# Kernel optimization log

Hardware: AMD Instinct MI355X
Metric: run time of the kernel (lower is better)

## Reference

```python
import jax, jax.numpy as jnp
import numpy as np

A = 4          # lanczos parameter
LUT = 1024     # LUT resolution; table has LUT+1 entries (torch.range is end-inclusive)
TAPS = 9
PAD = 4


def _lanczos_table():
    # delta_X = 1e-8 + i/1024, i = 0..1024  (matches torch.range(1e-8, 1.0, 1/1024))
    delta = jnp.float32(1e-08) + jnp.arange(LUT + 1, dtype=jnp.float32) / LUT  # (1025,)
    offs = jnp.arange(-PAD, PAD + 1, dtype=jnp.float32)[:, None]               # (9,1): row p -> delta + (p-4)
    t = delta[None, :] + offs                                                  # (9,1025)
    pi = jnp.float32(np.pi)
    return jnp.sin(t * pi) / (t * pi) * (jnp.sin(t * pi / A) / (t * pi / A))   # (9,1025)


def _resample_last_axis(x, sub, n_out):
    # x: (..., n_out) nearest-gathered signal; sub: (n_out,) fractional offsets in [0,1)
    pad = [(0, 0)] * (x.ndim - 1) + [(PAD, PAD)]
    xp = jnp.pad(x, pad, mode='reflect')                     # reflect pad by 4 on last axis
    idx = jnp.floor(sub * LUT).astype(jnp.int32)             # (n_out,) LUT index, 0..1023
    w = _lanczos_table()[:, idx]                             # (9, n_out) per-pixel tap weights
    # out[..., j] = sum_p w[p, j] * xp[..., j + p]
    return sum(w[p] * xp[..., p:p + n_out] for p in range(TAPS))


def reference(img, new_h, new_w):
    B, C, H, W = img.shape
    yv = jnp.arange(new_h, dtype=jnp.float32) * (H / new_h)   # torch.arange(0, H, H/H2)
    xv = jnp.arange(new_w, dtype=jnp.float32) * (W / new_w)
    yi = jnp.floor(yv).astype(jnp.int32)
    xi = jnp.floor(xv).astype(jnp.int32)
    ys = yv - yi                                              # fractional parts (separable)
    xs = xv - xi
    # nearest-neighbor gather img[:, :, y_init_up, x_init_up] -> (B, C, H2, W2)
    g = img[:, :, yi, :][:, :, :, xi]
    # horizontal Lanczos pass (unfold_x equivalent)
    hx = _resample_last_axis(g, xs, new_w)
    # vertical Lanczos pass (unfold_y equivalent), done on transposed view
    hy = _resample_last_axis(jnp.swapaxes(hx, 2, 3), ys, new_h)
    return jnp.swapaxes(hy, 2, 3)


def setup_inputs() -> dict:
    key = jax.random.key(0)
    img = jax.random.normal(key, (4, 2, 256, 256), dtype=jnp.float32)
    return {"img": img, "new_h": 2048, "new_w": 2048}
```

## Files before the change

### kernel.cpp

```cpp
#include <hip/hip_runtime.h>


#define WA0 0.0f
#define WA1 -0.03041110f
#define WA2 0.02753266f
#define WA3 -0.00827163f
#define WA4 1.00243180f
#define WA5 1.01040147f
#define WA6 0.97375330f
#define WA7 1.03080550f
#define WB0 1.0f
#define WB1 1.02991210f
#define WB2 0.97065798f
#define WB3 1.00472265f
#define WB4 -0.00765906f
#define WB5 -0.01652347f
#define WB6 0.02047608f
#define WB7 -0.03455115f
#define WS0 1.0f
#define WS1 0.99950100f
#define WS2 0.99819064f
#define WS3 0.99645102f
#define WS4 0.99477274f
#define WS5 0.99387800f
#define WS6 0.99422938f
#define WS7 0.99625435f

__global__ __launch_bounds__(512) void lanczos_up8_kernel(
    const float* __restrict__ img, float* __restrict__ out)
{
    int bid  = blockIdx.x;
    int t    = bid & 255;
    int bc   = bid >> 8;
    int v    = threadIdx.x;

    int P = v & 1;
    int m = v >> 1;

    bool eL = (v == 0);
    bool eR = (v == 511);

    float a0 = P ? WA4 : WA0, b0 = P ? WB4 : WB0;
    float a1 = P ? WA5 : WA1, b1 = P ? WB5 : WB1;
    float a2 = P ? WA6 : WA2, b2 = P ? WB6 : WB2;
    float a3 = P ? WA7 : WA3, b3 = P ? WB7 : WB3;
    if (eL) { a0 = WS0; a1 = WS1; a2 = WS2; a3 = WS3; b0 = b1 = b2 = b3 = 0.f; }
    if (eR) { a0 = WS4; a1 = WS5; a2 = WS6; a3 = WS7; b0 = b1 = b2 = b3 = 0.f; }

    int c0 = P ? m : m - 1;
    if (eL) c0 = 0;
    if (eR) c0 = 255;
    int c1 = (eL || eR) ? c0 : c0 + 1;

    int rm = t > 0   ? t - 1 : 0;
    int rp = t < 255 ? t + 1 : 255;

    const float* base = img + bc * 65536;
    float i00 = base[rm * 256 + c0], i01 = base[rm * 256 + c1];
    float i10 = base[t  * 256 + c0], i11 = base[t  * 256 + c1];
    float i20 = base[rp * 256 + c0], i21 = base[rp * 256 + c1];

    float h00 = a0*i00 + b0*i01, h01 = a1*i00 + b1*i01, h02 = a2*i00 + b2*i01, h03 = a3*i00 + b3*i01;
    float h10 = a0*i10 + b0*i11, h11 = a1*i10 + b1*i11, h12 = a2*i10 + b2*i11, h13 = a3*i10 + b3*i11;
    float h20 = a0*i20 + b0*i21, h21 = a1*i20 + b1*i21, h22 = a2*i20 + b2*i21, h23 = a3*i20 + b3*i21;

    bool eT = (t == 0);
    bool eB = (t == 255);

    float* op = out + (size_t)bc * (2048 * 2048)
                    + (size_t)(t << 3) * 2048 + (v << 2);

    float va, vb; float4 o;
#define EMIT(S, WAs, WBs, WSs, HX0,HX1,HX2,HX3, HY0,HY1,HY2,HY3, EDGE)   \
    va = (EDGE) ? WSs : WAs;  vb = (EDGE) ? 0.f : WBs;                   \
    o.x = va*HX0 + vb*HY0;  o.y = va*HX1 + vb*HY1;                       \
    o.z = va*HX2 + vb*HY2;  o.w = va*HX3 + vb*HY3;                       \
    *reinterpret_cast<float4*>(op + S * 2048) = o;

    EMIT(0, WA0, WB0, WS0, h00,h01,h02,h03, h10,h11,h12,h13, eT)
    EMIT(1, WA1, WB1, WS1, h00,h01,h02,h03, h10,h11,h12,h13, eT)
    EMIT(2, WA2, WB2, WS2, h00,h01,h02,h03, h10,h11,h12,h13, eT)
    EMIT(3, WA3, WB3, WS3, h00,h01,h02,h03, h10,h11,h12,h13, eT)
    EMIT(4, WA4, WB4, WS4, h10,h11,h12,h13, h20,h21,h22,h23, eB)
    EMIT(5, WA5, WB5, WS5, h10,h11,h12,h13, h20,h21,h22,h23, eB)
    EMIT(6, WA6, WB6, WS6, h10,h11,h12,h13, h20,h21,h22,h23, eB)
    EMIT(7, WA7, WB7, WS7, h10,h11,h12,h13, h20,h21,h22,h23, eB)
#undef EMIT
}

extern "C" void kernel_launch(void* const* d_in, const int* in_sizes, int n_in,
                              void* d_out, int out_size, void* d_ws, size_t ws_size,
                              hipStream_t stream) {
    const float* img = (const float*)d_in[0];
    float* out = (float*)d_out;
    dim3 grid(2048), block(512);
    hipLaunchKernelGGL(lanczos_up8_kernel, grid, block, 0, stream, img, out);
}
```

Measured before the change: 26.35 us.

## Remap threads so each wavefront writes one output row contiguously

Threads are reassigned so each wavefront owns one of the 8 output rows and loops over 8 column segments. Previously every thread wrote float4s across 8 rows. Now each store instruction covers a contiguous 1KB span of a single row, which is meant to improve write coalescing and reduce strided store streams. The cost is recomputing the vertical blend per column segment and issuing more, partly redundant, input loads per thread (mostly L1/L2 hits).

Result: slower. 27.23 us (+3.4%).

```diff
diff --git a/kernel.cpp b/kernel.cpp
--- a/kernel.cpp
+++ b/kernel.cpp
@@ -32,60 +32,54 @@
     int bid  = blockIdx.x;
     int t    = bid & 255;
     int bc   = bid >> 8;
-    int v    = threadIdx.x;
+    int tid  = threadIdx.x;
+    int lane = tid & 63;
+    int s    = tid >> 6;
 
-    int P = v & 1;
-    int m = v >> 1;
+    bool hi = (s >= 4);
+    float va = s==0?WA0: s==1?WA1: s==2?WA2: s==3?WA3: s==4?WA4: s==5?WA5: s==6?WA6: WA7;
+    float vb = s==0?WB0: s==1?WB1: s==2?WB2: s==3?WB3: s==4?WB4: s==5?WB5: s==6?WB6: WB7;
+    float ws = s==0?WS0: s==1?WS1: s==2?WS2: s==3?WS3: s==4?WS4: s==5?WS5: s==6?WS6: WS7;
+    bool eT = (t == 0)   && !hi;
+    bool eB = (t == 255) &&  hi;
+    if (eT || eB) { va = ws; vb = 0.f; }
+    int r0 = hi ? t : t - 1;  if (r0 < 0)   r0 = 0;
+    int r1 = r0 + 1;          if (r1 > 255) r1 = 255;
 
-    bool eL = (v == 0);
-    bool eR = (v == 511);
-
+    int P = lane & 1;
     float a0 = P ? WA4 : WA0, b0 = P ? WB4 : WB0;
     float a1 = P ? WA5 : WA1, b1 = P ? WB5 : WB1;
     float a2 = P ? WA6 : WA2, b2 = P ? WB6 : WB2;
     float a3 = P ? WA7 : WA3, b3 = P ? WB7 : WB3;
-    if (eL) { a0 = WS0; a1 = WS1; a2 = WS2; a3 = WS3; b0 = b1 = b2 = b3 = 0.f; }
-    if (eR) { a0 = WS4; a1 = WS5; a2 = WS6; a3 = WS7; b0 = b1 = b2 = b3 = 0.f; }
+    int cb = (lane >> 1) - 1 + P;
 
-    int c0 = P ? m : m - 1;
-    if (eL) c0 = 0;
-    if (eR) c0 = 255;
-    int c1 = (eL || eR) ? c0 : c0 + 1;
-
-    int rm = t > 0   ? t - 1 : 0;
-    int rp = t < 255 ? t + 1 : 255;
-
-    const float* base = img + bc * 65536;
-    float i00 = base[rm * 256 + c0], i01 = base[rm * 256 + c1];
-    float i10 = base[t  * 256 + c0], i11 = base[t  * 256 + c1];
-    float i20 = base[rp * 256 + c0], i21 = base[rp * 256 + c1];
-
-    float h00 = a0*i00 + b0*i01, h01 = a1*i00 + b1*i01, h02 = a2*i00 + b2*i01, h03 = a3*i00 + b3*i01;
-    float h10 = a0*i10 + b0*i11, h11 = a1*i10 + b1*i11, h12 = a2*i10 + b2*i11, h13 = a3*i10 + b3*i11;
-    float h20 = a0*i20 + b0*i21, h21 = a1*i20 + b1*i21, h22 = a2*i20 + b2*i21, h23 = a3*i20 + b3*i21;
-
-    bool eT = (t == 0);
-    bool eB = (t == 255);
+    const float* row0 = img + bc * 65536 + r0 * 256;
+    const float* row1 = img + bc * 65536 + r1 * 256;
 
     float* op = out + (size_t)bc * (2048 * 2048)
-                    + (size_t)(t << 3) * 2048 + (v << 2);
+                    + ((size_t)(t << 3) + s) * 2048 + (lane << 2);
 
-    float va, vb; float4 o;
-#define EMIT(S, WAs, WBs, WSs, HX0,HX1,HX2,HX3, HY0,HY1,HY2,HY3, EDGE)   \
-    va = (EDGE) ? WSs : WAs;  vb = (EDGE) ? 0.f : WBs;                   \
-    o.x = va*HX0 + vb*HY0;  o.y = va*HX1 + vb*HY1;                       \
-    o.z = va*HX2 + vb*HY2;  o.w = va*HX3 + vb*HY3;                       \
-    *reinterpret_cast<float4*>(op + S * 2048) = o;
-
-    EMIT(0, WA0, WB0, WS0, h00,h01,h02,h03, h10,h11,h12,h13, eT)
-    EMIT(1, WA1, WB1, WS1, h00,h01,h02,h03, h10,h11,h12,h13, eT)
-    EMIT(2, WA2, WB2, WS2, h00,h01,h02,h03, h10,h11,h12,h13, eT)
-    EMIT(3, WA3, WB3, WS3, h00,h01,h02,h03, h10,h11,h12,h13, eT)
-    EMIT(4, WA4, WB4, WS4, h10,h11,h12,h13, h20,h21,h22,h23, eB)
-    EMIT(5, WA5, WB5, WS5, h10,h11,h12,h13, h20,h21,h22,h23, eB)
-    EMIT(6, WA6, WB6, WS6, h10,h11,h12,h13, h20,h21,h22,h23, eB)
-    EMIT(7, WA7, WB7, WS7, h10,h11,h12,h13, h20,h21,h22,h23, eB)
-#undef EMIT
+    #pragma unroll
+    for (int st = 0; st < 8; ++st) {
+        int g  = (st << 6) | lane;
+        int c0 = cb + (st << 5);
+        int c1 = c0 + 1;
+        float A0=a0, A1=a1, A2=a2, A3=a3, B0=b0, B1=b1, B2=b2, B3=b3;
+        if (st == 0 && g == 0)   { A0=WS0; A1=WS1; A2=WS2; A3=WS3;
+                                   B0=B1=B2=B3=0.f; c0=0;   c1=0;   }
+        if (st == 7 && g == 511) { A0=WS4; A1=WS5; A2=WS6; A3=WS7;
+                                   B0=B1=B2=B3=0.f; c0=255; c1=255; }
+        float i0 = row0[c0], i1 = row0[c1];
+        float i2 = row1[c0], i3 = row1[c1];
+        float u = va * i0 + vb * i2;
+        float w = va * i1 + vb * i3;
+        float4 o;
+        o.x = A0 * u + B0 * w;
+        o.y = A1 * u + B1 * w;
+        o.z = A2 * u + B2 * w;
+        o.w = A3 * u + B3 * w;
+        *reinterpret_cast<float4*>(op + (st << 8)) = o;
+    }
 }
 
 extern "C" void kernel_launch(void* const* d_in, const int* in_sizes, int n_in,
```
